# Kernel optimization log

Hardware: AMD Instinct MI355X
Metric: run time of the kernel (lower is better)

Reference implementation:

```python
import jax, jax.numpy as jnp
import numpy as np

N_NODES = 512
STATE_DIM = 32
MESSAGE_DIM = 32
H_MSG = 64
H_RO = 64
N_STEPS = 5


def setup_inputs() -> dict:
    key = jax.random.key(0)
    ks = jax.random.split(key, 20)
    s = 0.01  # torch init: normal(0, 0.01) weights, zero biases
    d, m = STATE_DIM, MESSAGE_DIM
    inp = {
        "J": jax.random.normal(ks[0], (N_NODES, N_NODES), jnp.float32),
        "b": jax.random.normal(ks[1], (N_NODES,), jnp.float32),
        # message-passing MLP
        "mp_W1": jax.random.normal(ks[2], (H_MSG, 2 * d + 3), jnp.float32) * s,
        "mp_b1": jnp.zeros((H_MSG,), jnp.float32),
        "mp_W2": jax.random.normal(ks[3], (H_MSG, H_MSG), jnp.float32) * s,
        "mp_b2": jnp.zeros((H_MSG,), jnp.float32),
        "mp_W3": jax.random.normal(ks[4], (m, H_MSG), jnp.float32) * s,
        "mp_b3": jnp.zeros((m,), jnp.float32),
        # GRU (input = state_dim + message_dim, hidden = state_dim); gate order r,z,n
        "gru_Wih": jax.random.normal(ks[5], (3 * d, d + m), jnp.float32) * 0.1,
        "gru_Whh": jax.random.normal(ks[6], (3 * d, d), jnp.float32) * 0.1,
        "gru_bih": jax.random.normal(ks[7], (3 * d,), jnp.float32) * 0.1,
        "gru_bhh": jax.random.normal(ks[8], (3 * d,), jnp.float32) * 0.1,
        # readout MLP
        "r_W1": jax.random.normal(ks[9], (H_RO, d), jnp.float32) * s,
        "r_b1": jnp.zeros((H_RO,), jnp.float32),
        "r_W2": jax.random.normal(ks[10], (H_RO, H_RO), jnp.float32) * s,
        "r_b2": jnp.zeros((H_RO,), jnp.float32),
        "r_W3": jax.random.normal(ks[11], (2, H_RO), jnp.float32) * s,
        "r_b3": jnp.zeros((2,), jnp.float32),
    }
    return inp


def reference(J, b, mp_W1, mp_b1, mp_W2, mp_b2, mp_W3, mp_b3,
              gru_Wih, gru_Whh, gru_bih, gru_bhh,
              r_W1, r_b1, r_W2, r_b2, r_W3, r_b3):
    n = J.shape[0]
    d = gru_Whh.shape[1]
    # split first message-layer weight by input segments to avoid building [n,n,2d+3]
    Wi, Wj = mp_W1[:, :d], mp_W1[:, d:2 * d]          # [H, d]
    wJ, wbi, wbj = mp_W1[:, 2 * d], mp_W1[:, 2 * d + 1], mp_W1[:, 2 * d + 2]  # [H]

    def step(h, _):
        # pre[i, j, :] = W1 @ cat(h_i, h_j, J_ij, b_i, b_j) + b1
        pre = ((h @ Wi.T)[:, None, :] + (h @ Wj.T)[None, :, :]
               + J[:, :, None] * wJ + b[:, None, None] * wbi
               + b[None, :, None] * wbj + mp_b1)          # [n, n, H]
        m1 = jax.nn.relu(pre)
        m2 = jax.nn.relu(m1 @ mp_W2.T + mp_b2)            # [n, n, H]
        msg = jax.nn.relu(m2 @ mp_W3.T + mp_b3)           # [n, n, M]
        msg_sum = msg.sum(axis=0)                         # sum over senders i -> [n, M]
        # GRU cell over all nodes (torch GRU, gate order r,z,n)
        x = jnp.concatenate([h, msg_sum], axis=-1)        # [n, d+M]
        gi = x @ gru_Wih.T + gru_bih                      # [n, 3d]
        gh = h @ gru_Whh.T + gru_bhh                      # [n, 3d]
        i_r, i_z, i_n = jnp.split(gi, 3, axis=-1)
        h_r, h_z, h_n = jnp.split(gh, 3, axis=-1)
        r = jax.nn.sigmoid(i_r + h_r)
        z = jax.nn.sigmoid(i_z + h_z)
        n_g = jnp.tanh(i_n + r * h_n)
        h_new = (1.0 - z) * n_g + z * h
        return h_new, None

    h0 = jnp.zeros((n, d), J.dtype)
    h, _ = jax.lax.scan(step, h0, None, length=N_STEPS)
    y = jax.nn.relu(h @ r_W1.T + r_b1)
    y = jax.nn.relu(y @ r_W2.T + r_b2)
    y = jax.nn.relu(y @ r_W3.T + r_b3)                    # [n, 2]
    return jax.nn.sigmoid(y)
```

## Files before the change

kernel.cpp:

```cpp
#include <hip/hip_runtime.h>
#include <math.h>

#define NN 512
#define SD 32
#define HM 64

typedef _Float16 f16x8 __attribute__((ext_vector_type(8)));
typedef float floatx4 __attribute__((ext_vector_type(4)));
typedef unsigned uintx4 __attribute__((ext_vector_type(4)));

#define OFF_HBS   0
#define OFF_M2L   73728
#define OFF_MSUM  92160
#define OFF_HPREV 93184
#define OFF_HS    93440
#define OFF_MSG   93696
#define OFF_GI    93952
#define OFF_GH    94720
#define OFF_HJPS  95488
#define OFF_W65   96000
#define LDS_TOTAL 96256

__device__ __forceinline__ float sigmoidf_(float x) {
    return 1.0f / (1.0f + __expf(-x));
}
__device__ __forceinline__ unsigned pkrtz(float a, float b) {
    unsigned r;
    asm("v_cvt_pkrtz_f16_f32 %0, %1, %2" : "=v"(r) : "v"(a), "v"(b));
    return r;
}
__device__ __forceinline__ unsigned pk_add(unsigned a, unsigned b) {
    unsigned r;
    asm("v_pk_add_f16 %0, %1, %2" : "=v"(r) : "v"(a), "v"(b));
    return r;
}
__device__ __forceinline__ unsigned pk_fma(unsigned a, unsigned b, unsigned c) {
    unsigned r;
    asm("v_pk_fma_f16 %0, %1, %2, %3" : "=v"(r) : "v"(a), "v"(b), "v"(c));
    return r;
}
__device__ __forceinline__ unsigned pk_relu(unsigned a) {
    unsigned r, z = 0u;
    asm("v_pk_max_f16 %0, %1, %2" : "=v"(r) : "v"(a), "v"(z));
    return r;
}

struct SParams {
    const unsigned *hbR;  unsigned *hbW;
    const unsigned *hjR;  unsigned *hjW;
    const float *hR;      float *hW;
    float *JT, *W1T, *WihT, *WhhT, *rW1T, *rW2T;
    unsigned *w2p, *w3p, *wjp;
    const float *J, *mpW1, *mpb1, *mpW2, *mpb2, *mpW3, *mpb3;
    const float *Wih, *Whh, *bih, *bhh, *b;
    const float *rW1, *rW2, *rW3, *rb1, *rb2, *rb3;
    float *out;
    int hzero, rdout;
};

__global__ __launch_bounds__(512, 1) void step_kernel(SParams s)
{
    extern __shared__ __align__(16) char smem[];
    char* hbS = smem + OFF_HBS;
    float (*msum)[32]   = (float(*)[32])(smem + OFF_MSUM);
    float (*hPrevS)[32] = (float(*)[32])(smem + OFF_HPREV);
    float (*hS)[32]     = (float(*)[32])(smem + OFF_HS);
    float (*msgS)[32]   = (float(*)[32])(smem + OFF_MSG);
    float (*giS)[96]    = (float(*)[96])(smem + OFF_GI);
    float (*ghS)[96]    = (float(*)[96])(smem + OFF_GH);
    float (*hjpS)[64]   = (float(*)[64])(smem + OFF_HJPS);
    float* w65S         = (float*)(smem + OFF_W65);

    const int tid  = threadIdx.x;
    const int lane = tid & 63;
    const int wave = tid >> 6;
    const int nsel = wave >> 2;
    const int nw   = wave & 3;
    const int j    = blockIdx.x * 2 + nsel;
    const int q    = lane >> 4;
    const int c    = lane & 15;
    char* m2Lw = smem + OFF_M2L + wave * 2304;

    if (s.hzero) {
        if (blockIdx.x == 1) {
            for (int n = tid; n < 64 * 67; n += 512) {
                int cc = n / 67, d = n % 67;
                s.W1T[d * 64 + cc] = s.mpW1[n];
            }
        } else if (blockIdx.x == 2) {
            for (int n = tid; n < 96 * 64; n += 512)
                s.WihT[(n & 63) * 96 + (n >> 6)] = s.Wih[n];
        } else if (blockIdx.x == 3) {
            for (int n = tid; n < 96 * 32; n += 512)
                s.WhhT[(n & 31) * 96 + (n >> 5)] = s.Whh[n];
        } else if (blockIdx.x == 4) {
            for (int n = tid; n < 64 * 32; n += 512)
                s.rW1T[(n & 31) * 64 + (n >> 5)] = s.rW1[n];
            for (int n = tid; n < 64 * 64; n += 512)
                s.rW2T[(n & 63) * 64 + (n >> 6)] = s.rW2[n];
        } else if (blockIdx.x == 5 && tid < 64) {
            int l = tid, qq = l >> 4, cc = l & 15;
            for (int f = 0; f < 2; ++f)
                for (int t4 = 0; t4 < 4; ++t4) {
                    const float* src = s.mpW2 + (t4 * 16 + cc) * 64 + f * 32 + qq * 8;
                    unsigned* dst = s.w2p + ((f * 4 + t4) * 64 + l) * 4;
                    for (int i = 0; i < 4; ++i) dst[i] = pkrtz(src[2 * i], src[2 * i + 1]);
                }
            for (int f = 0; f < 2; ++f)
                for (int t2 = 0; t2 < 2; ++t2) {
                    const float* src = s.mpW3 + (t2 * 16 + cc) * 64 + f * 32 + qq * 8;
                    unsigned* dst = s.w3p + ((f * 2 + t2) * 64 + l) * 4;
                    for (int i = 0; i < 4; ++i) dst[i] = pkrtz(src[2 * i], src[2 * i + 1]);
                }
            for (int s2 = 0; s2 < 2; ++s2) {
                unsigned* dst = s.wjp + (s2 * 64 + l) * 4;
                for (int i = 0; i < 4; ++i) {
                    int r0 = qq * 8 + 2 * i + s2 * 32;
                    dst[i] = pkrtz(s.mpW1[r0 * 67 + 64], s.mpW1[(r0 + 1) * 67 + 64]);
                }
            }
        }
        if (tid < 64) w65S[tid] = s.mpW1[tid * 67 + 65];
        if (tid < 128) {
            int node = tid >> 6, cc = tid & 63;
            int jj = blockIdx.x * 2 + node;
            float bj = s.b[jj];
            hjpS[node][cc] = bj * s.mpW1[cc * 67 + 66] + s.mpb1[cc];
        }
        __syncthreads();
        {
            float bi = s.b[tid];
            unsigned* dst = (unsigned*)(hbS + tid * 144);
            #pragma unroll
            for (int k8 = 0; k8 < 8; ++k8) {
                uintx4 v;
                #pragma unroll
                for (int i = 0; i < 4; ++i) {
                    int k = k8 * 4 + i;
                    v[i] = pkrtz(bi * w65S[2 * k], bi * w65S[2 * k + 1]);
                }
                *(uintx4*)(dst + k8 * 4) = v;
            }
        }
    } else {
        uintx4 cr[8];
        const uintx4* gp = (const uintx4*)s.hbR;
        #pragma unroll
        for (int k = 0; k < 8; ++k) cr[k] = gp[k * 512 + tid];
        #pragma unroll
        for (int k = 0; k < 8; ++k) {
            int row = k * 64 + (tid >> 3);
            *(uintx4*)(hbS + row * 144 + (tid & 7) * 16) = cr[k];
        }
        if (tid < 64)
            hPrevS[tid >> 5][tid & 31] = s.hR[blockIdx.x * 64 + tid];
    }
    __syncthreads();

    f16x8 Aw2[2][4], Aw3[2][2];
    uintx4 wja, wjb, hja, hjb;
    if (s.hzero) {
        #pragma unroll
        for (int f = 0; f < 2; ++f)
            #pragma unroll
            for (int t4 = 0; t4 < 4; ++t4) {
                const float* src = s.mpW2 + (t4 * 16 + c) * 64 + f * 32 + q * 8;
                #pragma unroll
                for (int i = 0; i < 8; ++i) Aw2[f][t4][i] = (_Float16)src[i];
            }
        #pragma unroll
        for (int f = 0; f < 2; ++f)
            #pragma unroll
            for (int t2 = 0; t2 < 2; ++t2) {
                const float* src = s.mpW3 + (t2 * 16 + c) * 64 + f * 32 + q * 8;
                #pragma unroll
                for (int i = 0; i < 8; ++i) Aw3[f][t2][i] = (_Float16)src[i];
            }
        #pragma unroll
        for (int i = 0; i < 4; ++i) {
            wja[i] = pkrtz(s.mpW1[(q * 8 + 2 * i) * 67 + 64],
                           s.mpW1[(q * 8 + 2 * i + 1) * 67 + 64]);
            wjb[i] = pkrtz(s.mpW1[(q * 8 + 2 * i + 32) * 67 + 64],
                           s.mpW1[(q * 8 + 2 * i + 33) * 67 + 64]);
            hja[i] = pkrtz(hjpS[nsel][q * 8 + 2 * i], hjpS[nsel][q * 8 + 2 * i + 1]);
            hjb[i] = pkrtz(hjpS[nsel][q * 8 + 2 * i + 32], hjpS[nsel][q * 8 + 2 * i + 33]);
        }
    } else {
        #pragma unroll
        for (int f = 0; f < 2; ++f)
            #pragma unroll
            for (int t4 = 0; t4 < 4; ++t4)
                Aw2[f][t4] = __builtin_bit_cast(f16x8,
                    ((const uintx4*)s.w2p)[(f * 4 + t4) * 64 + lane]);
        #pragma unroll
        for (int f = 0; f < 2; ++f)
            #pragma unroll
            for (int t2 = 0; t2 < 2; ++t2)
                Aw3[f][t2] = __builtin_bit_cast(f16x8,
                    ((const uintx4*)s.w3p)[(f * 2 + t2) * 64 + lane]);
        wja = ((const uintx4*)s.wjp)[lane];
        wjb = ((const uintx4*)s.wjp)[64 + lane];
        hja = ((const uintx4*)s.hjR)[j * 8 + q];
        hjb = ((const uintx4*)s.hjR)[j * 8 + 4 + q];
    }

    floatx4 b2i[4], b3i[2];
    #pragma unroll
    for (int t4 = 0; t4 < 4; ++t4)
        #pragma unroll
        for (int r = 0; r < 4; ++r) b2i[t4][r] = s.mpb2[t4 * 16 + q * 4 + r];
    #pragma unroll
    for (int t2 = 0; t2 < 2; ++t2)
        #pragma unroll
        for (int r = 0; r < 4; ++r) b3i[t2][r] = s.mpb3[t2 * 16 + q * 4 + r];

    float jA, jB;
    if (s.hzero) {
        jA = s.J[((8 * q + nw) * 16 + c) * NN + j];
        jB = s.J[((8 * q + 4 + nw) * 16 + c) * NN + j];
        s.JT[j * NN + (8 * q + nw) * 16 + c] = jA;
        s.JT[j * NN + (8 * q + 4 + nw) * 16 + c] = jB;
    } else {
        jA = s.JT[j * NN + (8 * q + nw) * 16 + c];
        jB = s.JT[j * NN + (8 * q + 4 + nw) * 16 + c];
    }

    float accf[2][4];
    #pragma unroll
    for (int t2 = 0; t2 < 2; ++t2)
        #pragma unroll
        for (int r = 0; r < 4; ++r) accf[t2][r] = 0.0f;

    auto edge_group = [&](int G, float Jv) {
        const char* rb = hbS + (G * 16 + c) * 144;
        uintx4 vlo = *(const uintx4*)(rb + q * 16);
        uintx4 vhi = *(const uintx4*)(rb + 64 + q * 16);
        const unsigned Jp = pkrtz(Jv, Jv);

        uintx4 a0u, a1u;
        #pragma unroll
        for (int i = 0; i < 4; ++i) {
            a0u[i] = pk_relu(pk_fma(Jp, wja[i], pk_add(vlo[i], hja[i])));
            a1u[i] = pk_relu(pk_fma(Jp, wjb[i], pk_add(vhi[i], hjb[i])));
        }
        f16x8 B0 = __builtin_bit_cast(f16x8, a0u);
        f16x8 B1 = __builtin_bit_cast(f16x8, a1u);

        floatx4 c1[4];
        #pragma unroll
        for (int t4 = 0; t4 < 4; ++t4) {
            c1[t4] = __builtin_amdgcn_mfma_f32_16x16x32_f16(Aw2[0][t4], B0, b2i[t4], 0, 0, 0);
            c1[t4] = __builtin_amdgcn_mfma_f32_16x16x32_f16(Aw2[1][t4], B1, c1[t4], 0, 0, 0);
        }
        #pragma unroll
        for (int t4 = 0; t4 < 4; ++t4) {
            unsigned p0 = pkrtz(fmaxf(c1[t4][0], 0.f), fmaxf(c1[t4][1], 0.f));
            unsigned p1 = pkrtz(fmaxf(c1[t4][2], 0.f), fmaxf(c1[t4][3], 0.f));
            *(uint2*)(m2Lw + c * 144 + t4 * 32 + q * 8) = make_uint2(p0, p1);
        }
        uintx4 rlo = *(const uintx4*)(m2Lw + c * 144 + q * 16);
        uintx4 rhi = *(const uintx4*)(m2Lw + c * 144 + 64 + q * 16);
        f16x8 B2lo = __builtin_bit_cast(f16x8, rlo);
        f16x8 B2hi = __builtin_bit_cast(f16x8, rhi);

        floatx4 c2[2];
        #pragma unroll
        for (int t2 = 0; t2 < 2; ++t2) {
            c2[t2] = __builtin_amdgcn_mfma_f32_16x16x32_f16(Aw3[0][t2], B2lo, b3i[t2], 0, 0, 0);
            c2[t2] = __builtin_amdgcn_mfma_f32_16x16x32_f16(Aw3[1][t2], B2hi, c2[t2], 0, 0, 0);
        }
        #pragma unroll
        for (int t2 = 0; t2 < 2; ++t2)
            #pragma unroll
            for (int r = 0; r < 4; ++r)
                accf[t2][r] += fmaxf(c2[t2][r], 0.0f);
    };

    #pragma unroll
    for (int k = 0; k < 4; ++k) {
        edge_group(8 * k + nw,     __shfl(jA, k * 16 + c));
        edge_group(8 * k + 4 + nw, __shfl(jB, k * 16 + c));
    }

    #pragma unroll
    for (int m = 1; m < 16; m <<= 1)
        #pragma unroll
        for (int t2 = 0; t2 < 2; ++t2)
            #pragma unroll
            for (int r = 0; r < 4; ++r)
                accf[t2][r] += __shfl_xor(accf[t2][r], m);
    if (c == 0) {
        #pragma unroll
        for (int t2 = 0; t2 < 2; ++t2)
            #pragma unroll
            for (int r = 0; r < 4; ++r)
                msum[wave][t2 * 16 + q * 4 + r] = accf[t2][r];
    }
    __syncthreads();

    if (tid < 64) {
        int node = tid >> 5, d = tid & 31;
        msgS[node][d] = msum[node * 4 + 0][d] + msum[node * 4 + 1][d] +
                        msum[node * 4 + 2][d] + msum[node * 4 + 3][d];
    }
    __syncthreads();

    if (tid < 192) {
        int node = tid / 96, r = tid % 96;
        float a  = s.bih[r];
        float bb = s.bhh[r];
        if (!s.hzero) {
            #pragma unroll
            for (int k = 0; k < 32; ++k) {
                float hv = hPrevS[node][k];
                a  = fmaf(hv, s.WihT[k * 96 + r], a);
                bb = fmaf(hv, s.WhhT[k * 96 + r], bb);
            }
            #pragma unroll
            for (int k = 0; k < 32; ++k)
                a = fmaf(msgS[node][k], s.WihT[(32 + k) * 96 + r], a);
        } else {
            #pragma unroll
            for (int k = 0; k < 32; ++k)
                a = fmaf(msgS[node][k], s.Wih[r * 64 + 32 + k], a);
        }
        giS[node][r] = a; ghS[node][r] = bb;
    }
    __syncthreads();

    if (tid < 64) {
        int node = tid >> 5, d = tid & 31;
        float r  = sigmoidf_(giS[node][d] + ghS[node][d]);
        float z  = sigmoidf_(giS[node][32 + d] + ghS[node][32 + d]);
        float ng = tanhf(giS[node][64 + d] + r * ghS[node][64 + d]);
        float hold = s.hzero ? 0.0f : hPrevS[node][d];
        float hv = (1.0f - z) * ng + z * hold;
        hS[node][d] = hv;
        s.hW[blockIdx.x * 64 + tid] = hv;
    }
    __syncthreads();

    if (!s.rdout) {
        if (tid < 128) {
            int node = tid >> 6, cc = tid & 63;
            int jj = blockIdx.x * 2 + node;
            float bj = s.b[jj];
            float si, sj;
            if (s.hzero) {
                si = bj * s.mpW1[cc * 67 + 65];
                sj = bj * s.mpW1[cc * 67 + 66] + s.mpb1[cc];
                #pragma unroll
                for (int d = 0; d < 32; ++d) {
                    float hv = hS[node][d];
                    si = fmaf(hv, s.mpW1[cc * 67 + d], si);
                    sj = fmaf(hv, s.mpW1[cc * 67 + 32 + d], sj);
                }
            } else {
                si = bj * s.W1T[65 * 64 + cc];
                sj = bj * s.W1T[66 * 64 + cc] + s.mpb1[cc];
                #pragma unroll
                for (int d = 0; d < 32; ++d) {
                    float hv = hS[node][d];
                    si = fmaf(hv, s.W1T[d * 64 + cc], si);
                    sj = fmaf(hv, s.W1T[(32 + d) * 64 + cc], sj);
                }
            }
            float sip = __shfl(si, lane ^ 1);
            float sjp = __shfl(sj, lane ^ 1);
            if (!(cc & 1)) {
                s.hbW[jj * 32 + (cc >> 1)] = pkrtz(si, sip);
                s.hjW[jj * 32 + (cc >> 1)] = pkrtz(sj, sjp);
            }
        }
    } else {
        if (wave < 2) {
            int node = wave;
            int jj = blockIdx.x * 2 + node;
            float y1 = s.rb1[lane];
            #pragma unroll
            for (int k = 0; k < 32; ++k)
                y1 = fmaf(hS[node][k], s.rW1T[k * 64 + lane], y1);
            y1 = fmaxf(y1, 0.0f);
            float y2 = s.rb2[lane];
            #pragma unroll
            for (int k = 0; k < 64; ++k)
                y2 = fmaf(__shfl(y1, k), s.rW2T[k * 64 + lane], y2);
            y2 = fmaxf(y2, 0.0f);
            float y3 = (lane < 2) ? s.rb3[lane] : 0.0f;
            #pragma unroll
            for (int k = 0; k < 64; ++k) {
                float v = __shfl(y2, k);
                if (lane < 2) y3 = fmaf(v, s.rW3[lane * 64 + k], y3);
            }
            if (lane < 2) s.out[jj * 2 + lane] = sigmoidf_(y3);
        }
    }
}

extern "C" void kernel_launch(void* const* d_in, const int* in_sizes, int n_in,
                              void* d_out, int out_size, void* d_ws, size_t ws_size,
                              hipStream_t stream)
{
    float* ws = (float*)d_ws;

    SParams s;
    s.J    = (const float*)d_in[0];
    s.b    = (const float*)d_in[1];
    s.mpW1 = (const float*)d_in[2];
    s.mpb1 = (const float*)d_in[3];
    s.mpW2 = (const float*)d_in[4];
    s.mpb2 = (const float*)d_in[5];
    s.mpW3 = (const float*)d_in[6];
    s.mpb3 = (const float*)d_in[7];
    s.Wih  = (const float*)d_in[8];
    s.Whh  = (const float*)d_in[9];
    s.bih  = (const float*)d_in[10];
    s.bhh  = (const float*)d_in[11];
    s.rW1  = (const float*)d_in[12];
    s.rb1  = (const float*)d_in[13];
    s.rW2  = (const float*)d_in[14];
    s.rb2  = (const float*)d_in[15];
    s.rW3  = (const float*)d_in[16];
    s.rb3  = (const float*)d_in[17];
    s.out  = (float*)d_out;

    s.JT   = ws;
    s.W1T  = ws + 262144;
    s.WihT = ws + 266432;
    s.WhhT = ws + 272576;
    s.rW1T = ws + 275648;
    s.rW2T = ws + 277696;
    s.w2p  = (unsigned*)(ws + 281792);
    s.w3p  = (unsigned*)(ws + 283840);
    s.wjp  = (unsigned*)(ws + 284864);
    unsigned* hb0 = (unsigned*)(ws + 285376);
    unsigned* hb1 = (unsigned*)(ws + 301760);
    unsigned* hj0 = (unsigned*)(ws + 318144);
    unsigned* hj1 = (unsigned*)(ws + 334528);
    float*    h0  = ws + 350912;
    float*    h1  = ws + 367296;

    (void)hipFuncSetAttribute((const void*)step_kernel,
                              hipFuncAttributeMaxDynamicSharedMemorySize, LDS_TOTAL);

    for (int t = 0; t < 5; ++t) {
        s.hbR = (t & 1) ? hb1 : hb0;
        s.hbW = (t & 1) ? hb0 : hb1;
        s.hjR = (t & 1) ? hj1 : hj0;
        s.hjW = (t & 1) ? hj0 : hj1;
        s.hR  = (t & 1) ? h0 : h1;
        s.hW  = (t & 1) ? h1 : h0;
        s.hzero = (t == 0);
        s.rdout = (t == 4);
        step_kernel<<<dim3(256), dim3(512), LDS_TOTAL, stream>>>(s);
    }
}
```

Measured before the change: 153.1 us.

## Use one receiver node per 256-thread block and read hb from global directly

Restructures the step kernel so each block handles one receiver node with 4 waves instead of two nodes with 8 waves, launching 512 blocks with small static LDS rather than a ~96KB dynamic LDS staging of the whole hb table. Sender-side hb vectors are now read straight from global/L2 per edge group, and on the first step they are computed on the fly from b and packed W1 column weights instead of being materialised. This aims to raise occupancy (launch_bounds 256,4) and drop the per-block staging copy of 72KB into LDS, at the cost of repeated global/L2 reads of hb by every block.

```diff
diff --git a/kernel.cpp b/kernel.cpp
--- a/kernel.cpp
+++ b/kernel.cpp
@@ -8,18 +8,6 @@
 typedef _Float16 f16x8 __attribute__((ext_vector_type(8)));
 typedef float floatx4 __attribute__((ext_vector_type(4)));
 typedef unsigned uintx4 __attribute__((ext_vector_type(4)));
-
-#define OFF_HBS   0
-#define OFF_M2L   73728
-#define OFF_MSUM  92160
-#define OFF_HPREV 93184
-#define OFF_HS    93440
-#define OFF_MSG   93696
-#define OFF_GI    93952
-#define OFF_GH    94720
-#define OFF_HJPS  95488
-#define OFF_W65   96000
-#define LDS_TOTAL 96256
 
 __device__ __forceinline__ float sigmoidf_(float x) {
     return 1.0f / (1.0f + __expf(-x));
@@ -32,6 +20,11 @@
 __device__ __forceinline__ unsigned pk_add(unsigned a, unsigned b) {
     unsigned r;
     asm("v_pk_add_f16 %0, %1, %2" : "=v"(r) : "v"(a), "v"(b));
+    return r;
+}
+__device__ __forceinline__ unsigned pk_mul(unsigned a, unsigned b) {
+    unsigned r;
+    asm("v_pk_mul_f16 %0, %1, %2" : "=v"(r) : "v"(a), "v"(b));
     return r;
 }
 __device__ __forceinline__ unsigned pk_fma(unsigned a, unsigned b, unsigned c) {
@@ -58,45 +51,40 @@
     int hzero, rdout;
 };
 
-__global__ __launch_bounds__(512, 1) void step_kernel(SParams s)
+__global__ __launch_bounds__(256, 4) void step_kernel(SParams s)
 {
-    extern __shared__ __align__(16) char smem[];
-    char* hbS = smem + OFF_HBS;
-    float (*msum)[32]   = (float(*)[32])(smem + OFF_MSUM);
-    float (*hPrevS)[32] = (float(*)[32])(smem + OFF_HPREV);
-    float (*hS)[32]     = (float(*)[32])(smem + OFF_HS);
-    float (*msgS)[32]   = (float(*)[32])(smem + OFF_MSG);
-    float (*giS)[96]    = (float(*)[96])(smem + OFF_GI);
-    float (*ghS)[96]    = (float(*)[96])(smem + OFF_GH);
-    float (*hjpS)[64]   = (float(*)[64])(smem + OFF_HJPS);
-    float* w65S         = (float*)(smem + OFF_W65);
+    __shared__ __align__(16) char m2Lraw[4 * 2304];
+    __shared__ float msum[4][32];
+    __shared__ float hPrevS[32];
+    __shared__ float hS[32];
+    __shared__ float msgS[32];
+    __shared__ float giS[96], ghS[96];
+    __shared__ float hjpS[64];
 
     const int tid  = threadIdx.x;
     const int lane = tid & 63;
-    const int wave = tid >> 6;
-    const int nsel = wave >> 2;
-    const int nw   = wave & 3;
-    const int j    = blockIdx.x * 2 + nsel;
+    const int nw   = tid >> 6;
+    const int j    = blockIdx.x;
     const int q    = lane >> 4;
     const int c    = lane & 15;
-    char* m2Lw = smem + OFF_M2L + wave * 2304;
+    char* m2Lw = m2Lraw + nw * 2304;
 
     if (s.hzero) {
         if (blockIdx.x == 1) {
-            for (int n = tid; n < 64 * 67; n += 512) {
+            for (int n = tid; n < 64 * 67; n += 256) {
                 int cc = n / 67, d = n % 67;
                 s.W1T[d * 64 + cc] = s.mpW1[n];
             }
         } else if (blockIdx.x == 2) {
-            for (int n = tid; n < 96 * 64; n += 512)
+            for (int n = tid; n < 96 * 64; n += 256)
                 s.WihT[(n & 63) * 96 + (n >> 6)] = s.Wih[n];
         } else if (blockIdx.x == 3) {
-            for (int n = tid; n < 96 * 32; n += 512)
+            for (int n = tid; n < 96 * 32; n += 256)
                 s.WhhT[(n & 31) * 96 + (n >> 5)] = s.Whh[n];
         } else if (blockIdx.x == 4) {
-            for (int n = tid; n < 64 * 32; n += 512)
+            for (int n = tid; n < 64 * 32; n += 256)
                 s.rW1T[(n & 31) * 64 + (n >> 5)] = s.rW1[n];
-            for (int n = tid; n < 64 * 64; n += 512)
+            for (int n = tid; n < 64 * 64; n += 256)
                 s.rW2T[(n & 63) * 64 + (n >> 6)] = s.rW2[n];
         } else if (blockIdx.x == 5 && tid < 64) {
             int l = tid, qq = l >> 4, cc = l & 15;
@@ -120,45 +108,20 @@
                 }
             }
         }
-        if (tid < 64) w65S[tid] = s.mpW1[tid * 67 + 65];
-        if (tid < 128) {
-            int node = tid >> 6, cc = tid & 63;
-            int jj = blockIdx.x * 2 + node;
-            float bj = s.b[jj];
-            hjpS[node][cc] = bj * s.mpW1[cc * 67 + 66] + s.mpb1[cc];
+        if (tid < 64) {
+            float bj = s.b[j];
+            hjpS[tid] = bj * s.mpW1[tid * 67 + 66] + s.mpb1[tid];
         }
         __syncthreads();
-        {
-            float bi = s.b[tid];
-            unsigned* dst = (unsigned*)(hbS + tid * 144);
-            #pragma unroll
-            for (int k8 = 0; k8 < 8; ++k8) {
-                uintx4 v;
-                #pragma unroll
-                for (int i = 0; i < 4; ++i) {
-                    int k = k8 * 4 + i;
-                    v[i] = pkrtz(bi * w65S[2 * k], bi * w65S[2 * k + 1]);
-                }
-                *(uintx4*)(dst + k8 * 4) = v;
-            }
-        }
     } else {
-        uintx4 cr[8];
-        const uintx4* gp = (const uintx4*)s.hbR;
-        #pragma unroll
-        for (int k = 0; k < 8; ++k) cr[k] = gp[k * 512 + tid];
-        #pragma unroll
-        for (int k = 0; k < 8; ++k) {
-            int row = k * 64 + (tid >> 3);
-            *(uintx4*)(hbS + row * 144 + (tid & 7) * 16) = cr[k];
-        }
-        if (tid < 64)
-            hPrevS[tid >> 5][tid & 31] = s.hR[blockIdx.x * 64 + tid];
-    }
-    __syncthreads();
+        if (tid < 32) hPrevS[tid] = s.hR[j * 32 + tid];
+        __syncthreads();
+    }
 
     f16x8 Aw2[2][4], Aw3[2][2];
     uintx4 wja, wjb, hja, hjb;
+    unsigned w65pa[4], w65pb[4];
+    float bA = 0.f, bB = 0.f;
     if (s.hzero) {
         #pragma unroll
         for (int f = 0; f < 2; ++f)
@@ -182,9 +145,15 @@
                            s.mpW1[(q * 8 + 2 * i + 1) * 67 + 64]);
             wjb[i] = pkrtz(s.mpW1[(q * 8 + 2 * i + 32) * 67 + 64],
                            s.mpW1[(q * 8 + 2 * i + 33) * 67 + 64]);
-            hja[i] = pkrtz(hjpS[nsel][q * 8 + 2 * i], hjpS[nsel][q * 8 + 2 * i + 1]);
-            hjb[i] = pkrtz(hjpS[nsel][q * 8 + 2 * i + 32], hjpS[nsel][q * 8 + 2 * i + 33]);
-        }
+            w65pa[i] = pkrtz(s.mpW1[(q * 8 + 2 * i) * 67 + 65],
+                             s.mpW1[(q * 8 + 2 * i + 1) * 67 + 65]);
+            w65pb[i] = pkrtz(s.mpW1[(q * 8 + 2 * i + 32) * 67 + 65],
+                             s.mpW1[(q * 8 + 2 * i + 33) * 67 + 65]);
+            hja[i] = pkrtz(hjpS[q * 8 + 2 * i], hjpS[q * 8 + 2 * i + 1]);
+            hjb[i] = pkrtz(hjpS[q * 8 + 2 * i + 32], hjpS[q * 8 + 2 * i + 33]);
+        }
+        bA = s.b[(8 * q + nw) * 16 + c];
+        bB = s.b[(8 * q + 4 + nw) * 16 + c];
     } else {
         #pragma unroll
         for (int f = 0; f < 2; ++f)
@@ -231,10 +200,20 @@
         #pragma unroll
         for (int r = 0; r < 4; ++r) accf[t2][r] = 0.0f;
 
-    auto edge_group = [&](int G, float Jv) {
-        const char* rb = hbS + (G * 16 + c) * 144;
-        uintx4 vlo = *(const uintx4*)(rb + q * 16);
-        uintx4 vhi = *(const uintx4*)(rb + 64 + q * 16);
+    auto edge_group = [&](int G, float Jv, float bv) {
+        uintx4 vlo, vhi;
+        if (s.hzero) {
+            const unsigned Bp = pkrtz(bv, bv);
+            #pragma unroll
+            for (int i = 0; i < 4; ++i) {
+                vlo[i] = pk_mul(Bp, w65pa[i]);
+                vhi[i] = pk_mul(Bp, w65pb[i]);
+            }
+        } else {
+            const uintx4* rp = (const uintx4*)(s.hbR + (G * 16 + c) * 32);
+            vlo = rp[q];
+            vhi = rp[4 + q];
+        }
         const unsigned Jp = pkrtz(Jv, Jv);
 
         uintx4 a0u, a1u;
@@ -278,8 +257,8 @@
 
     #pragma unroll
     for (int k = 0; k < 4; ++k) {
-        edge_group(8 * k + nw,     __shfl(jA, k * 16 + c));
-        edge_group(8 * k + 4 + nw, __shfl(jB, k * 16 + c));
+        edge_group(8 * k + nw,     __shfl(jA, k * 16 + c), __shfl(bA, k * 16 + c));
+        edge_group(8 * k + 4 + nw, __shfl(jB, k * 16 + c), __shfl(bB, k * 16 + c));
     }
 
     #pragma unroll
@@ -294,64 +273,59 @@
         for (int t2 = 0; t2 < 2; ++t2)
             #pragma unroll
             for (int r = 0; r < 4; ++r)
-                msum[wave][t2 * 16 + q * 4 + r] = accf[t2][r];
+                msum[nw][t2 * 16 + q * 4 + r] = accf[t2][r];
     }
     __syncthreads();
 
-    if (tid < 64) {
-        int node = tid >> 5, d = tid & 31;
-        msgS[node][d] = msum[node * 4 + 0][d] + msum[node * 4 + 1][d] +
-                        msum[node * 4 + 2][d] + msum[node * 4 + 3][d];
-    }
+    if (tid < 32)
+        msgS[tid] = msum[0][tid] + msum[1][tid] + msum[2][tid] + msum[3][tid];
     __syncthreads();
 
-    if (tid < 192) {
-        int node = tid / 96, r = tid % 96;
+    if (tid < 96) {
+        int r = tid;
         float a  = s.bih[r];
         float bb = s.bhh[r];
         if (!s.hzero) {
             #pragma unroll
             for (int k = 0; k < 32; ++k) {
-                float hv = hPrevS[node][k];
+                float hv = hPrevS[k];
                 a  = fmaf(hv, s.WihT[k * 96 + r], a);
                 bb = fmaf(hv, s.WhhT[k * 96 + r], bb);
             }
             #pragma unroll
             for (int k = 0; k < 32; ++k)
-                a = fmaf(msgS[node][k], s.WihT[(32 + k) * 96 + r], a);
+                a = fmaf(msgS[k], s.WihT[(32 + k) * 96 + r], a);
         } else {
             #pragma unroll
             for (int k = 0; k < 32; ++k)
-                a = fmaf(msgS[node][k], s.Wih[r * 64 + 32 + k], a);
-        }
-        giS[node][r] = a; ghS[node][r] = bb;
+                a = fmaf(msgS[k], s.Wih[r * 64 + 32 + k], a);
+        }
+        giS[r] = a; ghS[r] = bb;
     }
     __syncthreads();
 
-    if (tid < 64) {
-        int node = tid >> 5, d = tid & 31;
-        float r  = sigmoidf_(giS[node][d] + ghS[node][d]);
-        float z  = sigmoidf_(giS[node][32 + d] + ghS[node][32 + d]);
-        float ng = tanhf(giS[node][64 + d] + r * ghS[node][64 + d]);
-        float hold = s.hzero ? 0.0f : hPrevS[node][d];
+    if (tid < 32) {
+        float r  = sigmoidf_(giS[tid] + ghS[tid]);
+        float z  = sigmoidf_(giS[32 + tid] + ghS[32 + tid]);
+        float ng = tanhf(giS[64 + tid] + r * ghS[64 + tid]);
+        float hold = s.hzero ? 0.0f : hPrevS[tid];
         float hv = (1.0f - z) * ng + z * hold;
-        hS[node][d] = hv;
-        s.hW[blockIdx.x * 64 + tid] = hv;
+        hS[tid] = hv;
+        s.hW[j * 32 + tid] = hv;
     }
     __syncthreads();
 
     if (!s.rdout) {
-        if (tid < 128) {
-            int node = tid >> 6, cc = tid & 63;
-            int jj = blockIdx.x * 2 + node;
-            float bj = s.b[jj];
+        if (tid < 64) {
+            int cc = tid;
+            float bj = s.b[j];
             float si, sj;
             if (s.hzero) {
                 si = bj * s.mpW1[cc * 67 + 65];
                 sj = bj * s.mpW1[cc * 67 + 66] + s.mpb1[cc];
                 #pragma unroll
                 for (int d = 0; d < 32; ++d) {
-                    float hv = hS[node][d];
+                    float hv = hS[d];
                     si = fmaf(hv, s.mpW1[cc * 67 + d], si);
                     sj = fmaf(hv, s.mpW1[cc * 67 + 32 + d], sj);
                 }
@@ -360,7 +334,7 @@
                 sj = bj * s.W1T[66 * 64 + cc] + s.mpb1[cc];
                 #pragma unroll
                 for (int d = 0; d < 32; ++d) {
-                    float hv = hS[node][d];
+                    float hv = hS[d];
                     si = fmaf(hv, s.W1T[d * 64 + cc], si);
                     sj = fmaf(hv, s.W1T[(32 + d) * 64 + cc], sj);
                 }
@@ -368,18 +342,16 @@
             float sip = __shfl(si, lane ^ 1);
             float sjp = __shfl(sj, lane ^ 1);
             if (!(cc & 1)) {
-                s.hbW[jj * 32 + (cc >> 1)] = pkrtz(si, sip);
-                s.hjW[jj * 32 + (cc >> 1)] = pkrtz(sj, sjp);
+                s.hbW[j * 32 + (cc >> 1)] = pkrtz(si, sip);
+                s.hjW[j * 32 + (cc >> 1)] = pkrtz(sj, sjp);
             }
         }
     } else {
-        if (wave < 2) {
-            int node = wave;
-            int jj = blockIdx.x * 2 + node;
+        if (nw == 0) {
             float y1 = s.rb1[lane];
             #pragma unroll
             for (int k = 0; k < 32; ++k)
-                y1 = fmaf(hS[node][k], s.rW1T[k * 64 + lane], y1);
+                y1 = fmaf(hS[k], s.rW1T[k * 64 + lane], y1);
             y1 = fmaxf(y1, 0.0f);
             float y2 = s.rb2[lane];
             #pragma unroll
@@ -392,7 +364,7 @@
                 float v = __shfl(y2, k);
                 if (lane < 2) y3 = fmaf(v, s.rW3[lane * 64 + k], y3);
             }
-            if (lane < 2) s.out[jj * 2 + lane] = sigmoidf_(y3);
+            if (lane < 2) s.out[j * 2 + lane] = sigmoidf_(y3);
         }
     }
 }
@@ -440,9 +412,6 @@
     float*    h0  = ws + 350912;
     float*    h1  = ws + 367296;
 
-    (void)hipFuncSetAttribute((const void*)step_kernel,
-                              hipFuncAttributeMaxDynamicSharedMemorySize, LDS_TOTAL);
-
     for (int t = 0; t < 5; ++t) {
         s.hbR = (t & 1) ? hb1 : hb0;
         s.hbW = (t & 1) ? hb0 : hb1;
@@ -452,6 +421,6 @@
         s.hW  = (t & 1) ? h1 : h0;
         s.hzero = (t == 0);
         s.rdout = (t == 4);
-        step_kernel<<<dim3(256), dim3(512), LDS_TOTAL, stream>>>(s);
-    }
-}
+        step_kernel<<<dim3(NN), dim3(256), 0, stream>>>(s);
+    }
+}
```

Result: slower. 229.3 us (+49.7%).

## Read sender h-projections directly from global instead of staging 72KB in LDS

Applied to the files above, without the earlier changes.

Each block no longer copies the full 512-row fp16 h-projection table into shared memory. Edge groups now load their rows straight from global (L2-resident) memory, and on the first step the b_i term is computed in registers with packed multiplies. This removes the bulk LDS staging and a block-wide barrier, and cuts LDS use from about 96KB to about 22KB with static allocation. In exchange, each wave issues redundant global loads, since the 256 blocks all reread the same table, and those loads may add latency inside the MFMA loop.

```diff
diff --git a/kernel.cpp b/kernel.cpp
--- a/kernel.cpp
+++ b/kernel.cpp
@@ -8,18 +8,6 @@
 typedef _Float16 f16x8 __attribute__((ext_vector_type(8)));
 typedef float floatx4 __attribute__((ext_vector_type(4)));
 typedef unsigned uintx4 __attribute__((ext_vector_type(4)));
-
-#define OFF_HBS   0
-#define OFF_M2L   73728
-#define OFF_MSUM  92160
-#define OFF_HPREV 93184
-#define OFF_HS    93440
-#define OFF_MSG   93696
-#define OFF_GI    93952
-#define OFF_GH    94720
-#define OFF_HJPS  95488
-#define OFF_W65   96000
-#define LDS_TOTAL 96256
 
 __device__ __forceinline__ float sigmoidf_(float x) {
     return 1.0f / (1.0f + __expf(-x));
@@ -32,6 +20,11 @@
 __device__ __forceinline__ unsigned pk_add(unsigned a, unsigned b) {
     unsigned r;
     asm("v_pk_add_f16 %0, %1, %2" : "=v"(r) : "v"(a), "v"(b));
+    return r;
+}
+__device__ __forceinline__ unsigned pk_mul(unsigned a, unsigned b) {
+    unsigned r;
+    asm("v_pk_mul_f16 %0, %1, %2" : "=v"(r) : "v"(a), "v"(b));
     return r;
 }
 __device__ __forceinline__ unsigned pk_fma(unsigned a, unsigned b, unsigned c) {
@@ -60,16 +53,13 @@
 
 __global__ __launch_bounds__(512, 1) void step_kernel(SParams s)
 {
-    extern __shared__ __align__(16) char smem[];
-    char* hbS = smem + OFF_HBS;
-    float (*msum)[32]   = (float(*)[32])(smem + OFF_MSUM);
-    float (*hPrevS)[32] = (float(*)[32])(smem + OFF_HPREV);
-    float (*hS)[32]     = (float(*)[32])(smem + OFF_HS);
-    float (*msgS)[32]   = (float(*)[32])(smem + OFF_MSG);
-    float (*giS)[96]    = (float(*)[96])(smem + OFF_GI);
-    float (*ghS)[96]    = (float(*)[96])(smem + OFF_GH);
-    float (*hjpS)[64]   = (float(*)[64])(smem + OFF_HJPS);
-    float* w65S         = (float*)(smem + OFF_W65);
+    __shared__ __align__(16) char m2Lraw[8 * 2304];
+    __shared__ float msum[8][32];
+    __shared__ float hPrevS[2][32];
+    __shared__ float hS[2][32];
+    __shared__ float msgS[2][32];
+    __shared__ float giS[2][96], ghS[2][96];
+    __shared__ float hjpS[2][64];
 
     const int tid  = threadIdx.x;
     const int lane = tid & 63;
@@ -79,7 +69,7 @@
     const int j    = blockIdx.x * 2 + nsel;
     const int q    = lane >> 4;
     const int c    = lane & 15;
-    char* m2Lw = smem + OFF_M2L + wave * 2304;
+    char* m2Lw = m2Lraw + wave * 2304;
 
     if (s.hzero) {
         if (blockIdx.x == 1) {
@@ -120,45 +110,22 @@
                 }
             }
         }
-        if (tid < 64) w65S[tid] = s.mpW1[tid * 67 + 65];
         if (tid < 128) {
             int node = tid >> 6, cc = tid & 63;
-            int jj = blockIdx.x * 2 + node;
-            float bj = s.b[jj];
+            float bj = s.b[blockIdx.x * 2 + node];
             hjpS[node][cc] = bj * s.mpW1[cc * 67 + 66] + s.mpb1[cc];
         }
         __syncthreads();
-        {
-            float bi = s.b[tid];
-            unsigned* dst = (unsigned*)(hbS + tid * 144);
-            #pragma unroll
-            for (int k8 = 0; k8 < 8; ++k8) {
-                uintx4 v;
-                #pragma unroll
-                for (int i = 0; i < 4; ++i) {
-                    int k = k8 * 4 + i;
-                    v[i] = pkrtz(bi * w65S[2 * k], bi * w65S[2 * k + 1]);
-                }
-                *(uintx4*)(dst + k8 * 4) = v;
-            }
-        }
     } else {
-        uintx4 cr[8];
-        const uintx4* gp = (const uintx4*)s.hbR;
-        #pragma unroll
-        for (int k = 0; k < 8; ++k) cr[k] = gp[k * 512 + tid];
-        #pragma unroll
-        for (int k = 0; k < 8; ++k) {
-            int row = k * 64 + (tid >> 3);
-            *(uintx4*)(hbS + row * 144 + (tid & 7) * 16) = cr[k];
-        }
         if (tid < 64)
             hPrevS[tid >> 5][tid & 31] = s.hR[blockIdx.x * 64 + tid];
-    }
-    __syncthreads();
+        __syncthreads();
+    }
 
     f16x8 Aw2[2][4], Aw3[2][2];
     uintx4 wja, wjb, hja, hjb;
+    unsigned w65pa[4], w65pb[4];
+    float bA = 0.f, bB = 0.f;
     if (s.hzero) {
         #pragma unroll
         for (int f = 0; f < 2; ++f)
@@ -182,9 +149,15 @@
                            s.mpW1[(q * 8 + 2 * i + 1) * 67 + 64]);
             wjb[i] = pkrtz(s.mpW1[(q * 8 + 2 * i + 32) * 67 + 64],
                            s.mpW1[(q * 8 + 2 * i + 33) * 67 + 64]);
+            w65pa[i] = pkrtz(s.mpW1[(q * 8 + 2 * i) * 67 + 65],
+                             s.mpW1[(q * 8 + 2 * i + 1) * 67 + 65]);
+            w65pb[i] = pkrtz(s.mpW1[(q * 8 + 2 * i + 32) * 67 + 65],
+                             s.mpW1[(q * 8 + 2 * i + 33) * 67 + 65]);
             hja[i] = pkrtz(hjpS[nsel][q * 8 + 2 * i], hjpS[nsel][q * 8 + 2 * i + 1]);
             hjb[i] = pkrtz(hjpS[nsel][q * 8 + 2 * i + 32], hjpS[nsel][q * 8 + 2 * i + 33]);
         }
+        bA = s.b[(8 * q + nw) * 16 + c];
+        bB = s.b[(8 * q + 4 + nw) * 16 + c];
     } else {
         #pragma unroll
         for (int f = 0; f < 2; ++f)
@@ -231,10 +204,20 @@
         #pragma unroll
         for (int r = 0; r < 4; ++r) accf[t2][r] = 0.0f;
 
-    auto edge_group = [&](int G, float Jv) {
-        const char* rb = hbS + (G * 16 + c) * 144;
-        uintx4 vlo = *(const uintx4*)(rb + q * 16);
-        uintx4 vhi = *(const uintx4*)(rb + 64 + q * 16);
+    auto edge_group = [&](int G, float Jv, float bv) {
+        uintx4 vlo, vhi;
+        if (s.hzero) {
+            const unsigned Bp = pkrtz(bv, bv);
+            #pragma unroll
+            for (int i = 0; i < 4; ++i) {
+                vlo[i] = pk_mul(Bp, w65pa[i]);
+                vhi[i] = pk_mul(Bp, w65pb[i]);
+            }
+        } else {
+            const uintx4* rp = (const uintx4*)(s.hbR + (G * 16 + c) * 32);
+            vlo = rp[q];
+            vhi = rp[4 + q];
+        }
         const unsigned Jp = pkrtz(Jv, Jv);
 
         uintx4 a0u, a1u;
@@ -278,8 +261,8 @@
 
     #pragma unroll
     for (int k = 0; k < 4; ++k) {
-        edge_group(8 * k + nw,     __shfl(jA, k * 16 + c));
-        edge_group(8 * k + 4 + nw, __shfl(jB, k * 16 + c));
+        edge_group(8 * k + nw,     __shfl(jA, k * 16 + c), __shfl(bA, k * 16 + c));
+        edge_group(8 * k + 4 + nw, __shfl(jB, k * 16 + c), __shfl(bB, k * 16 + c));
     }
 
     #pragma unroll
@@ -440,9 +423,6 @@
     float*    h0  = ws + 350912;
     float*    h1  = ws + 367296;
 
-    (void)hipFuncSetAttribute((const void*)step_kernel,
-                              hipFuncAttributeMaxDynamicSharedMemorySize, LDS_TOTAL);
-
     for (int t = 0; t < 5; ++t) {
         s.hbR = (t & 1) ? hb1 : hb0;
         s.hbW = (t & 1) ? hb0 : hb1;
@@ -452,6 +432,6 @@
         s.hW  = (t & 1) ? h1 : h0;
         s.hzero = (t == 0);
         s.rdout = (t == 4);
-        step_kernel<<<dim3(256), dim3(512), LDS_TOTAL, stream>>>(s);
-    }
-}
+        step_kernel<<<dim3(NN / 2), dim3(512), 0, stream>>>(s);
+    }
+}
```

Measured after the change: 156.4 us. 2.1% more time.
